# Performance work log

Hardware: AMD Instinct MI355X
Metric: run time of the kernel (lower is better)

Reference implementation:

```python
import jax, jax.numpy as jnp
import numpy as np

GRID = 128  # voxel grid extent
N_PTS = 100000


def _hash(c):
    c = c.astype(np.int64) + 16  # shift so offset-perturbed coords stay non-negative
    return (c[:, 0] * 512 + c[:, 1]) * 512 + c[:, 2]


def _offsets(vals):
    v = np.asarray(vals)
    return np.stack(np.meshgrid(v, v, v, indexing='ij'), axis=-1).reshape(-1, 3)


def _build_kmap(cin, cout, offsets):
    # For each kernel offset o, find pairs (in_idx, out_idx) with coord_in == coord_out + o.
    ki = _hash(cin)
    order = np.argsort(ki)
    ks = ki[order]
    ins, outs = [], []
    for o in offsets:
        q = _hash(cout + o[None, :])
        pos = np.searchsorted(ks, q)
        pc = np.clip(pos, 0, len(ks) - 1)
        found = ks[pc] == q
        ins.append(order[pc[found]])
        outs.append(np.nonzero(found)[0])
    K = len(offsets)
    P = max(1, max(len(a) for a in ins))
    in_idx = np.full((K, P), len(cin), np.int32)   # pad -> zero row of padded feats
    out_idx = np.full((K, P), len(cout), np.int32)  # pad -> dummy output row
    for k in range(K):
        in_idx[k, :len(ins[k])] = ins[k]
        out_idx[k, :len(outs[k])] = outs[k]
    return in_idx, out_idx


def _conv(x, W, in_idx, out_idx, n_out):
    # Minkowski sparse conv: per kernel offset, gather -> matmul -> scatter-add.
    xp = jnp.concatenate([x, jnp.zeros((1, x.shape[1]), x.dtype)], axis=0)
    out0 = jnp.zeros((n_out + 1, W.shape[-1]), x.dtype)

    def step(acc, kio):
        Wk, ik, ok = kio
        return acc.at[ok].add(xp[ik] @ Wk), None

    out, _ = jax.lax.scan(step, out0, (W, in_idx, out_idx))
    return out[:n_out]


def _bn(x, gamma, beta, eps=1e-5):
    # training-mode batch norm over the point dimension (biased variance)
    m = jnp.mean(x, axis=0)
    v = jnp.mean((x - m) ** 2, axis=0)
    return (x - m) * jax.lax.rsqrt(v + eps) * gamma + beta


def _forward(feats, W0, g0, b0,
             Ws1, gs1, bs1, Wa1, ga1, ba1, Wb1, gb1, bb1,
             Ws2, gs2, bs2, Wa2, ga2, ba2, Wb2, gb2, bb2, Wd2, gd2, bd2,
             Ws3, gs3, bs3, Wa3, ga3, ba3, Wb3, gb3, bb3, Wd3, gd3, bd3,
             c1, c2, c3,
             im0, om0, ims1, oms1, imb1, omb1, ims2, oms2, imb2, omb2,
             ims3, oms3, imb3, omb3):
    relu = jax.nn.relu
    n0, n1, n2, n3 = feats.shape[0], c1.shape[0], c2.shape[0], c3.shape[0]
    # stem: 5x5x5 conv + BN + ReLU (output coords == input coords)
    x = relu(_bn(_conv(feats, W0, im0, om0, n0), g0, b0))
    # level 1: stride-2 conv + BN + ReLU, then BasicBlock 64->64 (identity residual)
    x = relu(_bn(_conv(x, Ws1, ims1, oms1, n1), gs1, bs1))
    h = relu(_bn(_conv(x, Wa1, imb1, omb1, n1), ga1, ba1))
    h = _bn(_conv(h, Wb1, imb1, omb1, n1), gb1, bb1)
    y1 = relu(h + x)
    # level 2: stride-2 conv, then BasicBlock 64->128 (1x1 conv + BN residual)
    x = relu(_bn(_conv(y1, Ws2, ims2, oms2, n2), gs2, bs2))
    res = _bn(x @ Wd2, gd2, bd2)
    h = relu(_bn(_conv(x, Wa2, imb2, omb2, n2), ga2, ba2))
    h = _bn(_conv(h, Wb2, imb2, omb2, n2), gb2, bb2)
    y2 = relu(h + res)
    # level 3: stride-2 conv, then BasicBlock 128->256 (1x1 conv + BN residual)
    x = relu(_bn(_conv(y2, Ws3, ims3, oms3, n3), gs3, bs3))
    res = _bn(x @ Wd3, gd3, bd3)
    h = relu(_bn(_conv(x, Wa3, imb3, omb3, n3), ga3, ba3))
    h = _bn(_conv(h, Wb3, imb3, omb3, n3), gb3, bb3)
    y3 = relu(h + res)
    return (y1, y2, y3)


def setup_inputs() -> dict:
    rng = np.random.default_rng(0)
    c0 = np.unique(rng.integers(0, GRID, size=(N_PTS, 3)), axis=0).astype(np.int32)
    c1 = np.unique(c0 // 2 * 2, axis=0)
    c2 = np.unique(c1 // 4 * 4, axis=0)
    c3 = np.unique(c2 // 8 * 8, axis=0)
    im0, om0 = _build_kmap(c0, c0, _offsets([-2, -1, 0, 1, 2]))  # conv0 k=5, ts=1
    ims1, oms1 = _build_kmap(c0, c1, _offsets([0, 1]))           # stride-2, ts_in=1
    imb1, omb1 = _build_kmap(c1, c1, _offsets([-2, 0, 2]))       # k=3 at ts=2
    ims2, oms2 = _build_kmap(c1, c2, _offsets([0, 2]))
    imb2, omb2 = _build_kmap(c2, c2, _offsets([-4, 0, 4]))       # k=3 at ts=4
    ims3, oms3 = _build_kmap(c2, c3, _offsets([0, 4]))
    imb3, omb3 = _build_kmap(c3, c3, _offsets([-8, 0, 8]))       # k=3 at ts=8
    keys = iter(jax.random.split(jax.random.key(0), 16))

    def kai3(K, ci, co):  # kaiming_normal fan_out for [K, Cin, Cout] sparse kernels
        return jax.random.normal(next(keys), (K, ci, co), jnp.float32) * np.float32(np.sqrt(2.0 / (K * co)))

    def kai2(ci, co):
        return jax.random.normal(next(keys), (ci, co), jnp.float32) * np.float32(np.sqrt(2.0 / co))

    ones = lambda c: jnp.ones((c,), jnp.float32)
    zeros = lambda c: jnp.zeros((c,), jnp.float32)
    feats = jax.random.normal(next(keys), (c0.shape[0], 1), jnp.float32)
    return dict(
        feats=feats,
        W0=kai3(125, 1, 64), g0=ones(64), b0=zeros(64),
        Ws1=kai3(8, 64, 64), gs1=ones(64), bs1=zeros(64),
        Wa1=kai3(27, 64, 64), ga1=ones(64), ba1=zeros(64),
        Wb1=kai3(27, 64, 64), gb1=ones(64), bb1=zeros(64),
        Ws2=kai3(8, 64, 64), gs2=ones(64), bs2=zeros(64),
        Wa2=kai3(27, 64, 128), ga2=ones(128), ba2=zeros(128),
        Wb2=kai3(27, 128, 128), gb2=ones(128), bb2=zeros(128),
        Wd2=kai2(64, 128), gd2=ones(128), bd2=zeros(128),
        Ws3=kai3(8, 128, 128), gs3=ones(128), bs3=zeros(128),
        Wa3=kai3(27, 128, 256), ga3=ones(256), ba3=zeros(256),
        Wb3=kai3(27, 256, 256), gb3=ones(256), bb3=zeros(256),
        Wd3=kai2(128, 256), gd3=ones(256), bd3=zeros(256),
        c1=jnp.asarray(c1), c2=jnp.asarray(c2), c3=jnp.asarray(c3),
        im0=jnp.asarray(im0), om0=jnp.asarray(om0),
        ims1=jnp.asarray(ims1), oms1=jnp.asarray(oms1),
        imb1=jnp.asarray(imb1), omb1=jnp.asarray(omb1),
        ims2=jnp.asarray(ims2), oms2=jnp.asarray(oms2),
        imb2=jnp.asarray(imb2), omb2=jnp.asarray(omb2),
        ims3=jnp.asarray(ims3), oms3=jnp.asarray(oms3),
        imb3=jnp.asarray(imb3), omb3=jnp.asarray(omb3),
    )


def reference(feats, W0, g0, b0,
              Ws1, gs1, bs1, Wa1, ga1, ba1, Wb1, gb1, bb1,
              Ws2, gs2, bs2, Wa2, ga2, ba2, Wb2, gb2, bb2, Wd2, gd2, bd2,
              Ws3, gs3, bs3, Wa3, ga3, ba3, Wb3, gb3, bb3, Wd3, gd3, bd3,
              c1, c2, c3,
              im0, om0, ims1, oms1, imb1, omb1, ims2, oms2, imb2, omb2,
              ims3, oms3, imb3, omb3):
    return _forward(feats, W0, g0, b0,
                    Ws1, gs1, bs1, Wa1, ga1, ba1, Wb1, gb1, bb1,
                    Ws2, gs2, bs2, Wa2, ga2, ba2, Wb2, gb2, bb2, Wd2, gd2, bd2,
                    Ws3, gs3, bs3, Wa3, ga3, ba3, Wb3, gb3, bb3, Wd3, gd3, bd3,
                    c1, c2, c3,
                    im0, om0, ims1, oms1, imb1, omb1, ims2, oms2, imb2, omb2,
                    ims3, oms3, imb3, omb3)
```

## Files before the change

kernel.cpp:

```cpp
#include <hip/hip_runtime.h>
#include <hip/hip_bf16.h>
#include <cstdint>
#include <cstddef>

typedef __attribute__((ext_vector_type(8))) short sh8;
typedef __attribute__((ext_vector_type(4))) short sh4;
typedef __attribute__((ext_vector_type(4))) int ix4;
typedef __attribute__((ext_vector_type(16))) float floatx16;
typedef unsigned short ushort_t;

__device__ __forceinline__ void glds16(const ushort_t* g, ushort_t* l) {
  __builtin_amdgcn_global_load_lds(
      (const __attribute__((address_space(1))) void*)g,
      (__attribute__((address_space(3))) void*)l, 16, 0, 0);
}

__device__ __forceinline__ ushort_t f2bf_bits(float f) {
  __hip_bfloat16 b = __float2bfloat16(f);
  return __builtin_bit_cast(unsigned short, b);
}
__device__ __forceinline__ float bf2f(ushort_t u) {
  unsigned int x = ((unsigned int)u) << 16;
  return __builtin_bit_cast(float, x);
}

__global__ void build_ell_kernel(const int* __restrict__ in_idx,
                                 const int* __restrict__ out_idx,
                                 int K, int S, int P, int n_in, int n_out,
                                 int* __restrict__ ell) {
  int i = blockIdx.x * 256 + threadIdx.x;
  if (i >= K * P) return;
  int vin = in_idx[i];
  int vout = out_idx[i];
  if (vin < n_in && vout < n_out) {
    ell[(size_t)vout * S + (i / P)] = vin;
  }
}

__global__ void pack_u_kernel(const float* __restrict__ W,
                              __hip_bfloat16* __restrict__ Wp,
                              int K, int CSPLIT, int COUT, long total) {
  long i = (long)blockIdx.x * 256 + threadIdx.x;
  if (i >= total) return;
  int co = (int)(i % COUT);
  long t = i / COUT;
  int vch = (int)(t % 64);
  int vk = (int)(t / 64);
  int k = vk / CSPLIT;
  int ci = (vk % CSPLIT) * 64 + vch;
  int CIN = CSPLIT * 64;
  float v = (k < K) ? W[((long)k * CIN + ci) * COUT + co] : 0.f;
  Wp[(((long)vk * 8 + (vch >> 3)) * COUT + co) * 8 + (vch & 7)] =
      __float2bfloat16(v);
}

__global__ void pack_w0_kernel(const float* __restrict__ W,
                               __hip_bfloat16* __restrict__ Wp) {
  int i = blockIdx.x * 256 + threadIdx.x;
  if (i >= 128 * 64) return;
  int co = i & 63;
  int ki = i >> 6;
  float v = (ki < 125) ? W[ki * 64 + co] : 0.f;
  Wp[(((ki >> 4) * 64) + co) * 16 + (ki & 15)] = __float2bfloat16(v);
}

__global__ void f2bf_kernel(const float* __restrict__ x,
                            __hip_bfloat16* __restrict__ y, long n, long npad) {
  long i = (long)blockIdx.x * 256 + threadIdx.x;
  if (i >= npad) return;
  y[i] = __float2bfloat16(i < n ? x[i] : 0.f);
}

__global__ void reduce_parts_kernel(const float* __restrict__ part, int P,
                                    long total, ushort_t* __restrict__ out) {
  long i = (long)blockIdx.x * 256 + threadIdx.x;
  if (i >= total) return;
  float s = 0.f;
  for (int p = 0; p < P; ++p) s += part[(size_t)p * total + i];
  out[i] = f2bf_bits(s);
}

__global__ __launch_bounds__(256, 2) void conv0_mfma_kernel(
    const ushort_t* __restrict__ xpad, const ushort_t* __restrict__ Wp0,
    const int* __restrict__ ell, int n_out, ushort_t* __restrict__ out) {
  constexpr int STR = 152;
  __shared__ ushort_t xs[64 * STR];
  const int tid = threadIdx.x;
  const int lane = tid & 63;
  const int wv = tid >> 6;
  const int wm = wv & 1, wn = wv >> 1;
  const long m0 = (long)blockIdx.x * 64;
  const int row = tid >> 2;
  const int kk0 = (tid & 3) * 32;
  const long grow = m0 + row;

  if (grow < n_out) {
    const ix4* ep = (const ix4*)(ell + grow * 128 + kk0);
#pragma unroll
    for (int g = 0; g < 8; ++g) {
      ix4 e = ep[g];
      sh4 v;
#pragma unroll
      for (int j = 0; j < 4; ++j) {
        int ix = (e[j] < 0) ? n_out : e[j];
        v[j] = (short)xpad[ix];
      }
      *(sh4*)(&xs[row * STR + kk0 + g * 4]) = v;
    }
  } else {
    sh4 z = (sh4)(short)0;
#pragma unroll
    for (int g = 0; g < 8; ++g) *(sh4*)(&xs[row * STR + kk0 + g * 4]) = z;
  }
  __syncthreads();

  const int arow = wm * 32 + (lane & 31);
  const int koff = (lane >> 5) * 8;
  const int bcol = wn * 32 + (lane & 31);
  floatx16 acc = (floatx16)(0.0f);
#pragma unroll
  for (int kc = 0; kc < 8; ++kc) {
    sh8 a = *(const sh8*)(&xs[arow * STR + kc * 16 + koff]);
    sh8 b = *(const sh8*)(Wp0 + ((size_t)kc * 64 + bcol) * 16 + koff);
    acc = __builtin_amdgcn_mfma_f32_32x32x16_bf16(a, b, acc, 0, 0, 0);
  }
  const int lrow = (lane >> 5) * 4;
#pragma unroll
  for (int r = 0; r < 16; ++r) {
    long orow = m0 + wm * 32 + (r & 3) + 8 * (r >> 2) + lrow;
    if (orow < n_out) out[orow * 64 + bcol] = f2bf_bits(acc[r]);
  }
}

template <int CSPLIT, int CT, bool HASELL, bool BF16OUT>
__global__ __launch_bounds__(CT * 4, CT == 128 ? 4 : 3) void conv_u_kernel(
    const ushort_t* __restrict__ xb, const ushort_t* __restrict__ Wp,
    const int* __restrict__ ell, int S, int KI, int KP, int kdense,
    int n_out, int n_in, int COfull, int MB, int KS, int CS,
    void* __restrict__ outv) {
  constexpr int BLK = CT * 4;
  constexpr int NWN = CT / 32;
  constexpr int ASEG_PW = 16 / (BLK / 64);
  constexpr int BSEG_PW = (CT / 8) / (BLK / 64);
  constexpr int RW = CSPLIT * 64;
  __shared__ ushort_t Ab[2][128 * 64];
  __shared__ ushort_t Bb[2][8 * CT * 8];
  const int tid = threadIdx.x;
  const int lane = tid & 63;
  const int wv = tid >> 6;
  const int wm = wv / NWN, wn = wv % NWN;

  const int total = MB * KS * CS;
  const int l = blockIdx.x;
  const int q = total >> 3, r8 = total & 7;
  const int xcd = l & 7, pos = l >> 3;
  const int lp = (xcd < r8) ? (xcd * (q + 1) + pos)
                            : (r8 * (q + 1) + (xcd - r8) * q + pos);
  const int mblk = lp / (KS * CS);
  const int rem = lp - mblk * (KS * CS);
  const int yk = rem / CS;
  const int zc = rem - yk * CS;
  const long m0 = (long)mblk * 128;
  const int colbase = zc * CT;

  const int i0 = yk * KP;
  int cnt = KI - i0;
  if (cnt > KP) cnt = KP;

  floatx16 acc0 = (floatx16)(0.0f);
  floatx16 acc1 = (floatx16)(0.0f);

  auto loadEll = [&](int vk, int (&e)[ASEG_PW]) {
    if constexpr (HASELL) {
      const int kq = (CSPLIT == 1) ? vk : (vk / CSPLIT);
#pragma unroll
      for (int i = 0; i < ASEG_PW; ++i) {
        const int s = wv * ASEG_PW + i;
        const int r = s * 8 + (lane >> 3);
        long grow = m0 + r;
        long gc = grow < (long)(n_out - 1) ? grow : (long)(n_out - 1);
        e[i] = ell[gc * (long)S + kq];
      }
    }
  };

  auto stage = [&](int vk, ushort_t* A, ushort_t* B, int (&eRaw)[ASEG_PW]) {
    const int sub = (CSPLIT == 1) ? 0 : (vk % CSPLIT);
    const int kq = (CSPLIT == 1) ? vk : (vk / CSPLIT);
#pragma unroll
    for (int i = 0; i < ASEG_PW; ++i) {
      const int s = wv * ASEG_PW + i;
      const int r = s * 8 + (lane >> 3);
      const long grow = m0 + r;
      int v;
      if constexpr (HASELL) v = eRaw[i];
      else v = (kq < kdense) ? (int)grow : -1;
      if (grow >= (long)n_out) v = -1;
      const int e = (v < 0) ? n_in : v;
      const int c = lane & 7;
      const int lc = c ^ (r & 7);
      glds16(xb + (size_t)e * RW + sub * 64 + lc * 8, A + s * 512 + lane * 8);
    }
    const ushort_t* wb = Wp + (size_t)vk * 8 * COfull * 8;
#pragma unroll
    for (int i = 0; i < BSEG_PW; ++i) {
      const int s = wv * BSEG_PW + i;
      int lc, co;
      if (CT == 128) { lc = s >> 1; co = (s & 1) * 64 + lane; }
      else           { lc = s;      co = lane; }
      glds16(wb + ((size_t)lc * COfull + colbase + co) * 8,
             B + s * 512 + lane * 8);
    }
  };
  auto compute = [&](const ushort_t* A, const ushort_t* B) {
    const int r0 = wm * 64 + (lane & 31);
    const int h = lane >> 5;
    const int co = wn * 32 + (lane & 31);
#pragma unroll
    for (int kc = 0; kc < 4; ++kc) {
      const int lc = kc * 2 + h;
      const int pc = lc ^ (r0 & 7);
      sh8 a0 = *(const sh8*)(A + r0 * 64 + pc * 8);
      sh8 a1 = *(const sh8*)(A + (r0 + 32) * 64 + pc * 8);
      sh8 b = *(const sh8*)(B + ((size_t)lc * CT + co) * 8);
      acc0 = __builtin_amdgcn_mfma_f32_32x32x16_bf16(a0, b, acc0, 0, 0, 0);
      acc1 = __builtin_amdgcn_mfma_f32_32x32x16_bf16(a1, b, acc1, 0, 0, 0);
    }
  };

  constexpr int NWAIT = (ASEG_PW + BSEG_PW) + (HASELL ? ASEG_PW : 0);

  int eE[ASEG_PW] = {}, eO[ASEG_PW] = {};
  loadEll(i0, eE);
  stage(i0, Ab[0], Bb[0], eE);
  if (cnt > 1) loadEll(i0 + 1, eO);

#define CONV_ITER(J, P, SE, SO)                                                \
  if ((J) < cnt) {                                                             \
    __builtin_amdgcn_s_barrier();                                              \
    if ((J) + 1 < cnt) {                                                       \
      stage(i0 + (J) + 1, Ab[(P) ^ 1], Bb[(P) ^ 1], SO);                       \
      if ((J) + 2 < cnt) loadEll(i0 + (J) + 2, SE);                            \
      if constexpr (NWAIT == 4)                                                \
        asm volatile("s_waitcnt vmcnt(4)" ::: "memory");                       \
      else if constexpr (NWAIT == 6)                                           \
        asm volatile("s_waitcnt vmcnt(6)" ::: "memory");                       \
      else                                                                     \
        asm volatile("s_waitcnt vmcnt(10)" ::: "memory");                      \
    } else {                                                                   \
      asm volatile("s_waitcnt vmcnt(0)" ::: "memory");                         \
    }                                                                          \
    __builtin_amdgcn_s_barrier();                                              \
    __builtin_amdgcn_sched_barrier(0);                                         \
    compute(Ab[P], Bb[P]);                                                     \
  }

  for (int j = 0; j < cnt; j += 2) {
    CONV_ITER(j, 0, eE, eO)
    CONV_ITER(j + 1, 1, eO, eE)
  }
#undef CONV_ITER

  const int ccol = colbase + wn * 32 + (lane & 31);
  const int rb = wm * 64 + (lane >> 5) * 4;
  if constexpr (BF16OUT) {
    ushort_t* o = (ushort_t*)outv;
#pragma unroll
    for (int rr = 0; rr < 16; ++rr) {
      long row = m0 + rb + (rr & 3) + 8 * (rr >> 2);
      if (row < n_out) o[row * COfull + ccol] = f2bf_bits(acc0[rr]);
      long row1 = row + 32;
      if (row1 < n_out) o[row1 * COfull + ccol] = f2bf_bits(acc1[rr]);
    }
  } else {
    float* o = (float*)outv + (size_t)yk * ((size_t)n_out * COfull);
#pragma unroll
    for (int rr = 0; rr < 16; ++rr) {
      long row = m0 + rb + (rr & 3) + 8 * (rr >> 2);
      if (row < n_out) o[row * COfull + ccol] = acc0[rr];
      long row1 = row + 32;
      if (row1 < n_out) o[row1 * COfull + ccol] = acc1[rr];
    }
  }
}

template <int C>
__global__ void bn_reduce1_kernel(const ushort_t* __restrict__ x, int n,
                                  float* __restrict__ part) {
  constexpr int C4 = C / 4;
  constexpr int RL = 256 / C4;
  const int c4 = threadIdx.x % C4;
  const int rl = threadIdx.x / C4;
  float4 s = {0.f, 0.f, 0.f, 0.f}, ss = {0.f, 0.f, 0.f, 0.f};
  for (long row = (long)blockIdx.x * RL + rl; row < n;
       row += (long)gridDim.x * RL) {
    ushort4 u = *(const ushort4*)(x + row * C + c4 * 4);
    float v0 = bf2f(u.x), v1 = bf2f(u.y), v2 = bf2f(u.z), v3 = bf2f(u.w);
    s.x += v0; s.y += v1; s.z += v2; s.w += v3;
    ss.x += v0 * v0; ss.y += v1 * v1; ss.z += v2 * v2; ss.w += v3 * v3;
  }
  __shared__ float4 sh[512];
  sh[threadIdx.x] = s;
  sh[256 + threadIdx.x] = ss;
  __syncthreads();
  if (rl == 0) {
#pragma unroll
    for (int j = 1; j < RL; ++j) {
      float4 a = sh[j * C4 + c4];
      float4 b = sh[256 + j * C4 + c4];
      s.x += a.x; s.y += a.y; s.z += a.z; s.w += a.w;
      ss.x += b.x; ss.y += b.y; ss.z += b.z; ss.w += b.w;
    }
    *(float4*)(part + (size_t)blockIdx.x * 2 * C + c4 * 4) = s;
    *(float4*)(part + (size_t)blockIdx.x * 2 * C + C + c4 * 4) = ss;
  }
}

template <int C>
__global__ void bn_reduce2_kernel(const float* __restrict__ part, int G,
                                  float* __restrict__ stats) {
  const int c = blockIdx.x;
  const int g = threadIdx.x;
  __shared__ float sh[512];
  float s = 0.f, ss = 0.f;
  if (g < G) {
    s = part[(size_t)g * 2 * C + c];
    ss = part[(size_t)g * 2 * C + C + c];
  }
  sh[g] = s;
  sh[256 + g] = ss;
  __syncthreads();
#pragma unroll
  for (int off = 128; off > 0; off >>= 1) {
    if (g < off) {
      sh[g] += sh[g + off];
      sh[256 + g] += sh[256 + g + off];
    }
    __syncthreads();
  }
  if (g == 0) {
    stats[c] = sh[0];
    stats[C + c] = sh[256];
  }
}

template <int C, bool RELU, bool RES, bool WF32>
__global__ void bn_apply_kernel(const ushort_t* __restrict__ x,
                                const float* __restrict__ stats,
                                const float* __restrict__ gamma,
                                const float* __restrict__ beta,
                                const float* __restrict__ res,
                                long total4, float inv_n,
                                float* __restrict__ out,
                                ushort_t* __restrict__ outb, long padEnd4) {
  constexpr int C4 = C / 4;
  for (long i = (long)blockIdx.x * 256 + threadIdx.x; i < padEnd4;
       i += (long)gridDim.x * 256) {
    if (i >= total4) {
      if (outb) *(ushort4*)(outb + i * 4) = (ushort4){0, 0, 0, 0};
      continue;
    }
    const int c4 = (int)(i % C4);
    float4 sum = *(const float4*)(stats + c4 * 4);
    float4 sq = *(const float4*)(stats + C + c4 * 4);
    float4 g4 = *(const float4*)(gamma + c4 * 4);
    float4 b4 = *(const float4*)(beta + c4 * 4);
    ushort4 u = *(const ushort4*)(x + i * 4);
    float vin[4] = {bf2f(u.x), bf2f(u.y), bf2f(u.z), bf2f(u.w)};
    float4 r4 = {0.f, 0.f, 0.f, 0.f};
    if (RES) r4 = *(const float4*)(res + i * 4);
    float o[4];
#pragma unroll
    for (int j = 0; j < 4; ++j) {
      float m = ((const float*)&sum)[j] * inv_n;
      float var = ((const float*)&sq)[j] * inv_n - m * m;
      float sc = rsqrtf(var + 1e-5f) * ((const float*)&g4)[j];
      float val = (vin[j] - m) * sc + ((const float*)&b4)[j];
      if (RES) val += ((const float*)&r4)[j];
      if (RELU) val = fmaxf(val, 0.f);
      o[j] = val;
    }
    if (WF32) *(float4*)(out + i * 4) = (float4){o[0], o[1], o[2], o[3]};
    if (outb) {
      ushort4 w = {f2bf_bits(o[0]), f2bf_bits(o[1]), f2bf_bits(o[2]),
                   f2bf_bits(o[3])};
      *(ushort4*)(outb + i * 4) = w;
    }
  }
}


extern "C" void kernel_launch(void* const* d_in, const int* in_sizes, int n_in,
                              void* d_out, int out_size, void* d_ws,
                              size_t ws_size, hipStream_t stream) {
  const float* feats = (const float*)d_in[0];
  const float* W0  = (const float*)d_in[1];
  const float* g0  = (const float*)d_in[2];
  const float* b0  = (const float*)d_in[3];
  const float* Ws1 = (const float*)d_in[4];
  const float* gs1 = (const float*)d_in[5];
  const float* bs1 = (const float*)d_in[6];
  const float* Wa1 = (const float*)d_in[7];
  const float* ga1 = (const float*)d_in[8];
  const float* ba1 = (const float*)d_in[9];
  const float* Wb1 = (const float*)d_in[10];
  const float* gb1 = (const float*)d_in[11];
  const float* bb1 = (const float*)d_in[12];
  const float* Ws2 = (const float*)d_in[13];
  const float* gs2 = (const float*)d_in[14];
  const float* bs2 = (const float*)d_in[15];
  const float* Wa2 = (const float*)d_in[16];
  const float* ga2 = (const float*)d_in[17];
  const float* ba2 = (const float*)d_in[18];
  const float* Wb2 = (const float*)d_in[19];
  const float* gb2 = (const float*)d_in[20];
  const float* bb2 = (const float*)d_in[21];
  const float* Wd2 = (const float*)d_in[22];
  const float* gd2 = (const float*)d_in[23];
  const float* bd2 = (const float*)d_in[24];
  const float* Ws3 = (const float*)d_in[25];
  const float* gs3 = (const float*)d_in[26];
  const float* bs3 = (const float*)d_in[27];
  const float* Wa3 = (const float*)d_in[28];
  const float* ga3 = (const float*)d_in[29];
  const float* ba3 = (const float*)d_in[30];
  const float* Wb3 = (const float*)d_in[31];
  const float* gb3 = (const float*)d_in[32];
  const float* bb3 = (const float*)d_in[33];
  const float* Wd3 = (const float*)d_in[34];
  const float* gd3 = (const float*)d_in[35];
  const float* bd3 = (const float*)d_in[36];
  const int* im0  = (const int*)d_in[40];
  const int* om0  = (const int*)d_in[41];
  const int* ims1 = (const int*)d_in[42];
  const int* oms1 = (const int*)d_in[43];
  const int* imb1 = (const int*)d_in[44];
  const int* omb1 = (const int*)d_in[45];
  const int* ims2 = (const int*)d_in[46];
  const int* oms2 = (const int*)d_in[47];
  const int* imb2 = (const int*)d_in[48];
  const int* omb2 = (const int*)d_in[49];
  const int* ims3 = (const int*)d_in[50];
  const int* oms3 = (const int*)d_in[51];
  const int* imb3 = (const int*)d_in[52];
  const int* omb3 = (const int*)d_in[53];

  const int n0 = in_sizes[0];
  const int n1 = in_sizes[37] / 3;
  const int n2 = in_sizes[38] / 3;
  const int n3 = in_sizes[39] / 3;
  const int P0  = in_sizes[40] / 125;
  const int Ps1 = in_sizes[42] / 8;
  const int Pb1 = in_sizes[44] / 27;
  const int Ps2 = in_sizes[46] / 8;
  const int Pb2 = in_sizes[48] / 27;
  const int Ps3 = in_sizes[50] / 8;
  const int Pb3 = in_sizes[52] / 27;

  char* w = (char*)d_ws;
  auto carve = [&](size_t bytes) {
    char* p = w;
    w += (bytes + 255) & ~(size_t)255;
    return p;
  };
  int* ellS = (int*)carve((size_t)n0 * 128 * sizeof(int));
  int* ellB = (int*)carve((size_t)n1 * 28 * sizeof(int));
  float* part = (float*)carve((size_t)256 * 512 * sizeof(float));
  float* stats = (float*)carve((size_t)512 * sizeof(float));
  size_t capE = (size_t)n0 * 64 + 512;
  float* buf1 = (float*)carve(capE * sizeof(float));
  float* buf2 = (float*)carve(capE * sizeof(float));
  __hip_bfloat16* bbA = (__hip_bfloat16*)carve(capE * 2);
  __hip_bfloat16* bbB = (__hip_bfloat16*)carve(capE * 2);
  __hip_bfloat16* bbC = (__hip_bfloat16*)carve(capE * 2);
  ushort_t* cb1 = (ushort_t*)carve(capE * 2);
  ushort_t* cb2 = (ushort_t*)carve(capE * 2);
  ushort_t* cb3 = (ushort_t*)carve(capE * 2);
  __hip_bfloat16* xfeat = (__hip_bfloat16*)carve(((size_t)n0 + 1) * 2);

  auto packu = [&](const float* W, int K, int cin, int cout) {
    int csplit = cin / 64;
    long tot = (long)K * csplit * 64 * cout;
    __hip_bfloat16* Wp = (__hip_bfloat16*)carve((size_t)tot * 2);
    pack_u_kernel<<<(int)((tot + 255) / 256), 256, 0, stream>>>(
        W, Wp, K, csplit, cout, tot);
    return Wp;
  };
  __hip_bfloat16* Wp0 = (__hip_bfloat16*)carve((size_t)128 * 64 * 2);
  pack_w0_kernel<<<32, 256, 0, stream>>>(W0, Wp0);
  __hip_bfloat16* Ps1p = packu(Ws1, 8, 64, 64);
  __hip_bfloat16* Pa1p = packu(Wa1, 27, 64, 64);
  __hip_bfloat16* Pb1p = packu(Wb1, 27, 64, 64);
  __hip_bfloat16* Ps2p = packu(Ws2, 8, 64, 64);
  __hip_bfloat16* Pd2p = packu(Wd2, 1, 64, 128);
  __hip_bfloat16* Pa2p = packu(Wa2, 27, 64, 128);
  __hip_bfloat16* Pb2p = packu(Wb2, 27, 128, 128);
  __hip_bfloat16* Ps3p = packu(Ws3, 8, 128, 128);
  __hip_bfloat16* Pd3p = packu(Wd3, 1, 128, 256);
  __hip_bfloat16* Pa3p = packu(Wa3, 27, 128, 256);
  __hip_bfloat16* Pb3p = packu(Wb3, 27, 256, 256);

  size_t used = (size_t)(w - (char*)d_ws);
  float* pbuf = (float*)w;
  size_t pcap = (ws_size > used) ? (ws_size - used) / sizeof(float) : 0;

  f2bf_kernel<<<(int)((n0 + 256) / 256), 256, 0, stream>>>(feats, xfeat, n0,
                                                           n0 + 1);

  auto buildEll = [&](int* ellbuf, const int* im, const int* om, int K, int S,
                      int P, int nin, int nout) {
    hipMemsetAsync(ellbuf, 0xFF, (size_t)nout * S * sizeof(int), stream);
    int tot = K * P;
    build_ell_kernel<<<(tot + 255) / 256, 256, 0, stream>>>(im, om, K, S, P,
                                                            nin, nout, ellbuf);
  };

  auto convu = [&](const __hip_bfloat16* xb, const __hip_bfloat16* Wp,
                   const int* ellp, int S, int K, int kdense, int nout,
                   int nin, int cin, int cout, ushort_t* outc) {
    int csplit = cin / 64;
    int KIv = K * csplit;
    int CT = (cout >= 128) ? 128 : 64;
    int cs = cout / CT;
    int mb = (nout + 127) / 128;
    int tiles = mb * cs;
    int ks = 1;
    if (tiles < 512 && KIv > 1) {
      ks = (512 + tiles - 1) / tiles;
      if (ks > 8) ks = 8;
      if (ks > KIv) ks = KIv;
      size_t need = (size_t)nout * cout;
      int fit = need ? (int)(pcap / need) : 1;
      if (ks > fit) ks = fit;
      if (ks < 1) ks = 1;
    }
    int KP = (KIv + ks - 1) / ks;
    int ksE = (KIv + KP - 1) / KP;
    void* tgt = (ksE > 1) ? (void*)pbuf : (void*)outc;
    int gridx = mb * ksE * cs;
#define CU_CASE(CSV, CTV)                                                      \
  else if (csplit == CSV && CT == CTV) {                                       \
    if (ellp && ksE > 1)                                                       \
      conv_u_kernel<CSV, CTV, true, false><<<gridx, CTV * 4, 0, stream>>>(     \
          (const ushort_t*)xb, (const ushort_t*)Wp, ellp, S, KIv, KP, kdense,  \
          nout, nin, cout, mb, ksE, cs, tgt);                                  \
    else if (ellp)                                                             \
      conv_u_kernel<CSV, CTV, true, true><<<gridx, CTV * 4, 0, stream>>>(      \
          (const ushort_t*)xb, (const ushort_t*)Wp, ellp, S, KIv, KP, kdense,  \
          nout, nin, cout, mb, ksE, cs, tgt);                                  \
    else if (ksE > 1)                                                          \
      conv_u_kernel<CSV, CTV, false, false><<<gridx, CTV * 4, 0, stream>>>(    \
          (const ushort_t*)xb, (const ushort_t*)Wp, ellp, S, KIv, KP, kdense,  \
          nout, nin, cout, mb, ksE, cs, tgt);                                  \
    else                                                                       \
      conv_u_kernel<CSV, CTV, false, true><<<gridx, CTV * 4, 0, stream>>>(     \
          (const ushort_t*)xb, (const ushort_t*)Wp, ellp, S, KIv, KP, kdense,  \
          nout, nin, cout, mb, ksE, cs, tgt);                                  \
  }
    if (false) {}
    CU_CASE(1, 64)
    CU_CASE(1, 128)
    CU_CASE(2, 128)
    CU_CASE(4, 128)
#undef CU_CASE
    if (ksE > 1) {
      long total = (long)nout * cout;
      reduce_parts_kernel<<<(int)((total + 255) / 256), 256, 0, stream>>>(
          pbuf, ksE, total, outc);
    }
  };

  auto bn = [&](const ushort_t* x, int n, int C, const float* gamma,
                const float* beta, const float* res, bool relu, float* outp,
                __hip_bfloat16* outb) {
    const int G = 256;
    float invn = 1.0f / (float)n;
    long total4 = (long)n * C / 4;
    long padEnd4 = outb ? (total4 + C / 4) : total4;
    int agrid = (int)((padEnd4 + 255) / 256);
    if (agrid > 2048) agrid = 2048;
    ushort_t* outbu = (ushort_t*)outb;
#define BN_CASE(CC)                                                            \
  else if (C == CC) {                                                          \
    bn_reduce1_kernel<CC><<<G, 256, 0, stream>>>(x, n, part);                  \
    bn_reduce2_kernel<CC><<<CC, 256, 0, stream>>>(part, G, stats);             \
    if (res && relu)                                                           \
      bn_apply_kernel<CC, true, true, true><<<agrid, 256, 0, stream>>>(        \
          x, stats, gamma, beta, res, total4, invn, outp, outbu, padEnd4);     \
    else if (relu && outp)                                                     \
      bn_apply_kernel<CC, true, false, true><<<agrid, 256, 0, stream>>>(       \
          x, stats, gamma, beta, nullptr, total4, invn, outp, outbu,           \
          padEnd4);                                                            \
    else if (relu)                                                             \
      bn_apply_kernel<CC, true, false, false><<<agrid, 256, 0, stream>>>(      \
          x, stats, gamma, beta, nullptr, total4, invn, nullptr, outbu,        \
          padEnd4);                                                            \
    else                                                                       \
      bn_apply_kernel<CC, false, false, true><<<agrid, 256, 0, stream>>>(      \
          x, stats, gamma, beta, nullptr, total4, invn, outp, outbu,           \
          padEnd4);                                                            \
  }
    if (false) {}
    BN_CASE(64)
    BN_CASE(128)
    BN_CASE(256)
#undef BN_CASE
  };

  float* y1 = (float*)d_out;
  float* y2 = y1 + (size_t)n1 * 64;
  float* y3 = y2 + (size_t)n2 * 128;

  buildEll(ellS, im0, om0, 125, 128, P0, n0, n0);
  conv0_mfma_kernel<<<(n0 + 63) / 64, 256, 0, stream>>>(
      (const ushort_t*)xfeat, (const ushort_t*)Wp0, ellS, n0, cb1);
  bn(cb1, n0, 64, g0, b0, nullptr, true, nullptr, bbA);

  buildEll(ellS, ims1, oms1, 8, 8, Ps1, n0, n1);
  convu(bbA, Ps1p, ellS, 8, 8, 0, n1, n0, 64, 64, cb2);
  bn(cb2, n1, 64, gs1, bs1, nullptr, true, buf2, bbB);
  buildEll(ellB, imb1, omb1, 27, 28, Pb1, n1, n1);
  convu(bbB, Pa1p, ellB, 28, 27, 0, n1, n1, 64, 64, cb3);
  bn(cb3, n1, 64, ga1, ba1, nullptr, true, nullptr, bbC);
  convu(bbC, Pb1p, ellB, 28, 27, 0, n1, n1, 64, 64, cb1);
  bn(cb1, n1, 64, gb1, bb1, buf2, true, y1, bbA);

  buildEll(ellS, ims2, oms2, 8, 8, Ps2, n1, n2);
  convu(bbA, Ps2p, ellS, 8, 8, 0, n2, n1, 64, 64, cb2);
  bn(cb2, n2, 64, gs2, bs2, nullptr, true, nullptr, bbB);
  convu(bbB, Pd2p, nullptr, 1, 1, 1, n2, n2, 64, 128, cb3);
  bn(cb3, n2, 128, gd2, bd2, nullptr, false, buf1, nullptr);
  buildEll(ellB, imb2, omb2, 27, 28, Pb2, n2, n2);
  convu(bbB, Pa2p, ellB, 28, 27, 0, n2, n2, 64, 128, cb2);
  bn(cb2, n2, 128, ga2, ba2, nullptr, true, nullptr, bbC);
  convu(bbC, Pb2p, ellB, 28, 27, 0, n2, n2, 128, 128, cb3);
  bn(cb3, n2, 128, gb2, bb2, buf1, true, y2, bbA);

  buildEll(ellS, ims3, oms3, 8, 8, Ps3, n2, n3);
  convu(bbA, Ps3p, ellS, 8, 8, 0, n3, n2, 128, 128, cb1);
  bn(cb1, n3, 128, gs3, bs3, nullptr, true, nullptr, bbB);
  convu(bbB, Pd3p, nullptr, 1, 1, 1, n3, n3, 128, 256, cb2);
  bn(cb2, n3, 256, gd3, bd3, nullptr, false, buf2, nullptr);
  buildEll(ellB, imb3, omb3, 27, 28, Pb3, n3, n3);
  convu(bbB, Pa3p, ellB, 28, 27, 0, n3, n3, 128, 256, cb1);
  bn(cb1, n3, 256, ga3, ba3, nullptr, true, nullptr, bbC);
  convu(bbC, Pb3p, ellB, 28, 27, 0, n3, n3, 256, 256, cb2);
  bn(cb2, n3, 256, gb3, bb3, buf2, true, y3, nullptr);
}
```

Baseline: 636.5 us.

## Store split-K partials in bf16, single-buffer weights, raise occupancy bounds

Split-K partial sums are now written as bf16 instead of fp32, which halves partial-buffer traffic and lets larger split factors fit in the workspace. The weight tile in shared memory is no longer double-buffered: it is loaded synchronously each iteration right after the barrier. That frees LDS so the launch bounds can ask for more blocks per CU, but the weight load is no longer overlapped with compute. The bf16 partials lose precision in the reduction, and the changed vmcnt waits must match the new load counts.

```diff
diff --git a/kernel.cpp b/kernel.cpp
--- a/kernel.cpp
+++ b/kernel.cpp
@@ -71,12 +71,12 @@
   y[i] = __float2bfloat16(i < n ? x[i] : 0.f);
 }
 
-__global__ void reduce_parts_kernel(const float* __restrict__ part, int P,
+__global__ void reduce_parts_kernel(const ushort_t* __restrict__ part, int P,
                                     long total, ushort_t* __restrict__ out) {
   long i = (long)blockIdx.x * 256 + threadIdx.x;
   if (i >= total) return;
   float s = 0.f;
-  for (int p = 0; p < P; ++p) s += part[(size_t)p * total + i];
+  for (int p = 0; p < P; ++p) s += bf2f(part[(size_t)p * total + i]);
   out[i] = f2bf_bits(s);
 }
 
@@ -132,19 +132,19 @@
   }
 }
 
-template <int CSPLIT, int CT, bool HASELL, bool BF16OUT>
-__global__ __launch_bounds__(CT * 4, CT == 128 ? 4 : 3) void conv_u_kernel(
+template <int CSPLIT, int CT, bool HASELL>
+__global__ __launch_bounds__(CT * 4, CT == 128 ? 6 : 4) void conv_u_kernel(
     const ushort_t* __restrict__ xb, const ushort_t* __restrict__ Wp,
     const int* __restrict__ ell, int S, int KI, int KP, int kdense,
     int n_out, int n_in, int COfull, int MB, int KS, int CS,
-    void* __restrict__ outv) {
+    ushort_t* __restrict__ out) {
   constexpr int BLK = CT * 4;
   constexpr int NWN = CT / 32;
   constexpr int ASEG_PW = 16 / (BLK / 64);
   constexpr int BSEG_PW = (CT / 8) / (BLK / 64);
   constexpr int RW = CSPLIT * 64;
   __shared__ ushort_t Ab[2][128 * 64];
-  __shared__ ushort_t Bb[2][8 * CT * 8];
+  __shared__ ushort_t Bb[8 * CT * 8];
   const int tid = threadIdx.x;
   const int lane = tid & 63;
   const int wv = tid >> 6;
@@ -166,6 +166,7 @@
   const int i0 = yk * KP;
   int cnt = KI - i0;
   if (cnt > KP) cnt = KP;
+  out += (size_t)yk * ((size_t)n_out * COfull);
 
   floatx16 acc0 = (floatx16)(0.0f);
   floatx16 acc1 = (floatx16)(0.0f);
@@ -184,7 +185,7 @@
     }
   };
 
-  auto stage = [&](int vk, ushort_t* A, ushort_t* B, int (&eRaw)[ASEG_PW]) {
+  auto stageA = [&](int vk, ushort_t* A, int (&eRaw)[ASEG_PW]) {
     const int sub = (CSPLIT == 1) ? 0 : (vk % CSPLIT);
     const int kq = (CSPLIT == 1) ? vk : (vk / CSPLIT);
 #pragma unroll
@@ -201,6 +202,8 @@
       const int lc = c ^ (r & 7);
       glds16(xb + (size_t)e * RW + sub * 64 + lc * 8, A + s * 512 + lane * 8);
     }
+  };
+  auto stageB = [&](int vk) {
     const ushort_t* wb = Wp + (size_t)vk * 8 * COfull * 8;
 #pragma unroll
     for (int i = 0; i < BSEG_PW; ++i) {
@@ -209,10 +212,10 @@
       if (CT == 128) { lc = s >> 1; co = (s & 1) * 64 + lane; }
       else           { lc = s;      co = lane; }
       glds16(wb + ((size_t)lc * COfull + colbase + co) * 8,
-             B + s * 512 + lane * 8);
-    }
-  };
-  auto compute = [&](const ushort_t* A, const ushort_t* B) {
+             Bb + s * 512 + lane * 8);
+    }
+  };
+  auto compute = [&](const ushort_t* A) {
     const int r0 = wm * 64 + (lane & 31);
     const int h = lane >> 5;
     const int co = wn * 32 + (lane & 31);
@@ -222,37 +225,38 @@
       const int pc = lc ^ (r0 & 7);
       sh8 a0 = *(const sh8*)(A + r0 * 64 + pc * 8);
       sh8 a1 = *(const sh8*)(A + (r0 + 32) * 64 + pc * 8);
-      sh8 b = *(const sh8*)(B + ((size_t)lc * CT + co) * 8);
+      sh8 b = *(const sh8*)(Bb + ((size_t)lc * CT + co) * 8);
       acc0 = __builtin_amdgcn_mfma_f32_32x32x16_bf16(a0, b, acc0, 0, 0, 0);
       acc1 = __builtin_amdgcn_mfma_f32_32x32x16_bf16(a1, b, acc1, 0, 0, 0);
     }
   };
 
-  constexpr int NWAIT = (ASEG_PW + BSEG_PW) + (HASELL ? ASEG_PW : 0);
+  constexpr int NWAIT = ASEG_PW + (HASELL ? ASEG_PW : 0);
 
   int eE[ASEG_PW] = {}, eO[ASEG_PW] = {};
   loadEll(i0, eE);
-  stage(i0, Ab[0], Bb[0], eE);
+  stageA(i0, Ab[0], eE);
   if (cnt > 1) loadEll(i0 + 1, eO);
 
 #define CONV_ITER(J, P, SE, SO)                                                \
   if ((J) < cnt) {                                                             \
-    __builtin_amdgcn_s_barrier();                                              \
+    __builtin_amdgcn_s_barrier();    \
+    stageB(i0 + (J));                                                          \
     if ((J) + 1 < cnt) {                                                       \
-      stage(i0 + (J) + 1, Ab[(P) ^ 1], Bb[(P) ^ 1], SO);                       \
+      stageA(i0 + (J) + 1, Ab[(P) ^ 1], SO);                                   \
       if ((J) + 2 < cnt) loadEll(i0 + (J) + 2, SE);                            \
-      if constexpr (NWAIT == 4)                                                \
+      if constexpr (NWAIT == 2)                                                \
+        asm volatile("s_waitcnt vmcnt(2)" ::: "memory");                       \
+      else if constexpr (NWAIT == 4)                                           \
         asm volatile("s_waitcnt vmcnt(4)" ::: "memory");                       \
-      else if constexpr (NWAIT == 6)                                           \
-        asm volatile("s_waitcnt vmcnt(6)" ::: "memory");                       \
       else                                                                     \
-        asm volatile("s_waitcnt vmcnt(10)" ::: "memory");                      \
+        asm volatile("s_waitcnt vmcnt(8)" ::: "memory");                       \
     } else {                                                                   \
       asm volatile("s_waitcnt vmcnt(0)" ::: "memory");                         \
     }                                                                          \
-    __builtin_amdgcn_s_barrier();                                              \
+    __builtin_amdgcn_s_barrier();          \
     __builtin_amdgcn_sched_barrier(0);                                         \
-    compute(Ab[P], Bb[P]);                                                     \
+    compute(Ab[P]);                                                            \
   }
 
   for (int j = 0; j < cnt; j += 2) {
@@ -263,24 +267,12 @@
 
   const int ccol = colbase + wn * 32 + (lane & 31);
   const int rb = wm * 64 + (lane >> 5) * 4;
-  if constexpr (BF16OUT) {
-    ushort_t* o = (ushort_t*)outv;
-#pragma unroll
-    for (int rr = 0; rr < 16; ++rr) {
-      long row = m0 + rb + (rr & 3) + 8 * (rr >> 2);
-      if (row < n_out) o[row * COfull + ccol] = f2bf_bits(acc0[rr]);
-      long row1 = row + 32;
-      if (row1 < n_out) o[row1 * COfull + ccol] = f2bf_bits(acc1[rr]);
-    }
-  } else {
-    float* o = (float*)outv + (size_t)yk * ((size_t)n_out * COfull);
-#pragma unroll
-    for (int rr = 0; rr < 16; ++rr) {
-      long row = m0 + rb + (rr & 3) + 8 * (rr >> 2);
-      if (row < n_out) o[row * COfull + ccol] = acc0[rr];
-      long row1 = row + 32;
-      if (row1 < n_out) o[row1 * COfull + ccol] = acc1[rr];
-    }
+#pragma unroll
+  for (int rr = 0; rr < 16; ++rr) {
+    long row = m0 + rb + (rr & 3) + 8 * (rr >> 2);
+    if (row < n_out) out[row * COfull + ccol] = f2bf_bits(acc0[rr]);
+    long row1 = row + 32;
+    if (row1 < n_out) out[row1 * COfull + ccol] = f2bf_bits(acc1[rr]);
   }
 }
 
@@ -501,8 +493,8 @@
   __hip_bfloat16* Pb3p = packu(Wb3, 27, 256, 256);
 
   size_t used = (size_t)(w - (char*)d_ws);
-  float* pbuf = (float*)w;
-  size_t pcap = (ws_size > used) ? (ws_size - used) / sizeof(float) : 0;
+  ushort_t* pbufU = (ushort_t*)w;
+  size_t pcapU = (ws_size > used) ? (ws_size - used) / 2 : 0;
 
   f2bf_kernel<<<(int)((n0 + 256) / 256), 256, 0, stream>>>(feats, xfeat, n0,
                                                            n0 + 1);
@@ -530,30 +522,22 @@
       if (ks > 8) ks = 8;
       if (ks > KIv) ks = KIv;
       size_t need = (size_t)nout * cout;
-      int fit = need ? (int)(pcap / need) : 1;
+      int fit = need ? (int)(pcapU / need) : 1;
       if (ks > fit) ks = fit;
       if (ks < 1) ks = 1;
     }
     int KP = (KIv + ks - 1) / ks;
     int ksE = (KIv + KP - 1) / KP;
-    void* tgt = (ksE > 1) ? (void*)pbuf : (void*)outc;
+    ushort_t* tgt = (ksE > 1) ? pbufU : outc;
     int gridx = mb * ksE * cs;
 #define CU_CASE(CSV, CTV)                                                      \
   else if (csplit == CSV && CT == CTV) {                                       \
-    if (ellp && ksE > 1)                                                       \
-      conv_u_kernel<CSV, CTV, true, false><<<gridx, CTV * 4, 0, stream>>>(     \
-          (const ushort_t*)xb, (const ushort_t*)Wp, ellp, S, KIv, KP, kdense,  \
-          nout, nin, cout, mb, ksE, cs, tgt);                                  \
-    else if (ellp)                                                             \
-      conv_u_kernel<CSV, CTV, true, true><<<gridx, CTV * 4, 0, stream>>>(      \
-          (const ushort_t*)xb, (const ushort_t*)Wp, ellp, S, KIv, KP, kdense,  \
-          nout, nin, cout, mb, ksE, cs, tgt);                                  \
-    else if (ksE > 1)                                                          \
-      conv_u_kernel<CSV, CTV, false, false><<<gridx, CTV * 4, 0, stream>>>(    \
+    if (ellp)                                                                  \
+      conv_u_kernel<CSV, CTV, true><<<gridx, CTV * 4, 0, stream>>>(            \
           (const ushort_t*)xb, (const ushort_t*)Wp, ellp, S, KIv, KP, kdense,  \
           nout, nin, cout, mb, ksE, cs, tgt);                                  \
     else                                                                       \
-      conv_u_kernel<CSV, CTV, false, true><<<gridx, CTV * 4, 0, stream>>>(     \
+      conv_u_kernel<CSV, CTV, false><<<gridx, CTV * 4, 0, stream>>>(           \
           (const ushort_t*)xb, (const ushort_t*)Wp, ellp, S, KIv, KP, kdense,  \
           nout, nin, cout, mb, ksE, cs, tgt);                                  \
   }
@@ -566,7 +550,7 @@
     if (ksE > 1) {
       long total = (long)nout * cout;
       reduce_parts_kernel<<<(int)((total + 255) / 256), 256, 0, stream>>>(
-          pbuf, ksE, total, outc);
+          pbufU, ksE, total, outc);
     }
   };
 
```

Result: faster. 612.2 us (-3.8%).
